# Performance work log

Measured on AMD Instinct MI355X. Metric: run time of the kernel, lower is better.

The kernel has to match this reference:

```python
import jax, jax.numpy as jnp
import numpy as np

N = 4096
NFEAT = 256
NHID1 = 64
NHID2 = 32
NCLASS = 8
NHEADS = 4
NADJ = 2
ALPHA = 0.2  # leaky relu slope
NEG = -9e15


def setup_inputs() -> dict:
    key = jax.random.key(0)
    ks = jax.random.split(key, 14)
    x = jax.random.normal(ks[0], (N, NFEAT), jnp.float32)
    adj = (jax.random.uniform(ks[1], (NADJ, N, N)) < 0.01).astype(jnp.float32)
    adj = jnp.maximum(adj, jnp.eye(N, dtype=jnp.float32)[None])
    s = 0.05
    W1 = jax.random.normal(ks[2], (NADJ, NHEADS, NFEAT, NHID1), jnp.float32) * s
    a1 = jax.random.normal(ks[3], (NADJ, NHEADS, 2, NHID1), jnp.float32) * s
    W2 = jax.random.normal(ks[4], (NADJ, NHEADS, NHID1, NHID2), jnp.float32) * s
    a2 = jax.random.normal(ks[5], (NADJ, NHEADS, 2, NHID2), jnp.float32) * s
    Wi1 = jax.random.normal(ks[6], (NHID1 * NHEADS, NHID1), jnp.float32) * s
    bi1 = jnp.zeros((NHID1,), jnp.float32)
    Wi2 = jax.random.normal(ks[7], (NHID2 * NHEADS, NCLASS), jnp.float32) * s
    bi2 = jnp.zeros((NCLASS,), jnp.float32)
    Wf = jax.random.normal(ks[8], (NCLASS * NADJ, NCLASS), jnp.float32) * s
    bf = jnp.zeros((NCLASS,), jnp.float32)
    return {"x": x, "adj": adj, "W1": W1, "a1": a1, "W2": W2, "a2": a2,
            "Wi1": Wi1, "bi1": bi1, "Wi2": Wi2, "bi2": bi2, "Wf": Wf, "bf": bf}


def gat_multihead(x, adj_i, W, a):
    # x: [n, f]; adj_i: [n, n]; W: [h, f, o]; a: [h, 2, o]
    Wh = jnp.einsum('nf,hfo->hno', x, W)                 # [h, n, o]
    f_src = jnp.einsum('hno,ho->hn', Wh, a[:, 0])        # [h, n]
    f_dst = jnp.einsum('hno,ho->hn', Wh, a[:, 1])        # [h, n]
    e = jax.nn.leaky_relu(f_src[:, :, None] + f_dst[:, None, :], ALPHA)
    e = jnp.where(adj_i[None] > 0, e, NEG)               # masked scores [h, n, n]
    att = jax.nn.softmax(e, axis=-1)
    h = jnp.einsum('hnm,hmo->hno', att, Wh)              # aggregate
    h = jax.nn.elu(h)                                     # concat=True -> elu
    n = x.shape[0]
    return jnp.transpose(h, (1, 0, 2)).reshape(n, -1)     # [n, h*o]


def reference(x, adj, W1, a1, W2, a2, Wi1, bi1, Wi2, bi2, Wf, bf):
    outs = []
    for i in range(NADJ):  # small fixed loop over adjacency graphs
        xi = gat_multihead(x, adj[i], W1[i], a1[i])
        xi = jax.nn.elu(xi @ Wi1 + bi1)
        xi = gat_multihead(xi, adj[i], W2[i], a2[i])
        xi = jax.nn.elu(xi @ Wi2 + bi2)
        outs.append(xi)
    out = jnp.concatenate(outs, axis=1) @ Wf + bf         # [n, nclass]
    l1_loss = jnp.mean(jnp.abs(Wf))
    return jax.nn.log_softmax(out, axis=1), l1_loss
```

## Files before the change

### kernel.cpp

```cpp
#include <hip/hip_runtime.h>
#include <hip/hip_bf16.h>

#define NN 4096
#define NFEAT 256
#define NHID1 64
#define NHID2 32
#define NCLASS 8
#define NHEADS 4
#define NADJ 2
#define CAP 128

__global__ __launch_bounds__(256) void build_edges(const float* __restrict__ adj,
                                                   int* __restrict__ eidx,
                                                   int* __restrict__ ecnt) {
  const int wave = threadIdx.x >> 6;
  const int lane = threadIdx.x & 63;
  const int r = blockIdx.x * 4 + wave;
  const float4* row = (const float4*)(adj + (size_t)r * NN);
  int* out = eidx + (size_t)r * CAP;
  int base = 0;
  for (int c = 0; c < NN; c += 256) {
    const float4 v = row[(c >> 2) + lane];
    const int j0 = c + lane * 4;
    const float vt[4] = {v.x, v.y, v.z, v.w};
#pragma unroll
    for (int t = 0; t < 4; ++t) {
      const bool hit = vt[t] > 0.f;
      const unsigned long long m = __ballot(hit);
      if (hit) {
        const int pos = base + __popcll(m & ((1ull << lane) - 1ull));
        if (pos < CAP) out[pos] = j0 + t;
      }
      base += __popcll(m);
    }
  }
  if (lane == 0) ecnt[r] = base < CAP ? base : CAP;
}

template <int KDIM, int NDIM, int RPTY, int ACT, int COEF>
__global__ __launch_bounds__(256) void gemm_tile(
    const float* __restrict__ A, const float* __restrict__ B,
    const float* __restrict__ bias, float* __restrict__ C,
    const float* __restrict__ av, float* __restrict__ fsrc,
    float* __restrict__ fdst,
    size_t asG, size_t bsH, size_t bsG, size_t csH, size_t csG) {
  constexpr int KT = 32;
  constexpr int TX = NDIM / 4;
  constexpr int TY = 256 / TX;
  constexpr int BR = TY * RPTY;
  const int g = blockIdx.z, h = blockIdx.y;
  const int gh = g * NHEADS + h;
  A += (size_t)g * asG;
  B += (size_t)g * bsG + (size_t)h * bsH;
  C += (size_t)g * csG + (size_t)h * csH;
  __shared__ float AsT[KT][BR + 4];
  __shared__ float Bs[KT][NDIM + 4];
  const int tid = threadIdx.x;
  const int tx = tid % TX, ty = tid / TX;
  const int row0b = blockIdx.x * BR;
  const int c0 = tx * 4;
  float acc[RPTY][4];
#pragma unroll
  for (int i = 0; i < RPTY; ++i)
#pragma unroll
    for (int j = 0; j < 4; ++j) acc[i][j] = 0.f;

  for (int kt = 0; kt < KDIM; kt += KT) {
    __syncthreads();
    for (int i = tid; i < BR * (KT / 4); i += 256) {
      const int r = i / (KT / 4), e = i % (KT / 4);
      const float4 v = *(const float4*)(A + (size_t)(row0b + r) * KDIM + kt + e * 4);
      AsT[e * 4 + 0][r] = v.x;
      AsT[e * 4 + 1][r] = v.y;
      AsT[e * 4 + 2][r] = v.z;
      AsT[e * 4 + 3][r] = v.w;
    }
    for (int i = tid; i < KT * (NDIM / 4); i += 256) {
      const int k = i / (NDIM / 4), cc = i % (NDIM / 4);
      *(float4*)&Bs[k][cc * 4] = *(const float4*)(B + (size_t)(kt + k) * NDIM + cc * 4);
    }
    __syncthreads();
#pragma unroll
    for (int k = 0; k < KT; ++k) {
      float a4[RPTY];
      if constexpr (RPTY == 4) {
        const float4 t = *(const float4*)&AsT[k][ty * 4];
        a4[0] = t.x; a4[1] = t.y; a4[2] = t.z; a4[3] = t.w;
      } else {
        const float2 t = *(const float2*)&AsT[k][ty * 2];
        a4[0] = t.x; a4[1] = t.y;
      }
      const float4 bv = *(const float4*)&Bs[k][c0];
      const float b4[4] = {bv.x, bv.y, bv.z, bv.w};
#pragma unroll
      for (int i = 0; i < RPTY; ++i)
#pragma unroll
        for (int j = 0; j < 4; ++j) acc[i][j] += a4[i] * b4[j];
    }
  }
  float b4[4] = {0.f, 0.f, 0.f, 0.f};
  if (bias) {
    const float4 bb = *(const float4*)&bias[c0];
    b4[0] = bb.x; b4[1] = bb.y; b4[2] = bb.z; b4[3] = bb.w;
  }
#pragma unroll
  for (int i = 0; i < RPTY; ++i) {
    const int row = row0b + ty * RPTY + i;
    float4 o;
    float* op = (float*)&o;
#pragma unroll
    for (int j = 0; j < 4; ++j) {
      float v = acc[i][j] + b4[j];
      if (ACT == 1) v = v > 0.f ? v : (__expf(v) - 1.f);
      op[j] = v;
    }
    *(float4*)&C[(size_t)row * NDIM + c0] = o;
  }
  if constexpr (COEF) {
    const float* ag = av + (size_t)gh * 2 * NDIM;
    float aS[4], aD[4];
#pragma unroll
    for (int j = 0; j < 4; ++j) { aS[j] = ag[c0 + j]; aD[j] = ag[NDIM + c0 + j]; }
#pragma unroll
    for (int i = 0; i < RPTY; ++i) {
      float s = 0.f, d = 0.f;
#pragma unroll
      for (int j = 0; j < 4; ++j) { s += acc[i][j] * aS[j]; d += acc[i][j] * aD[j]; }
#pragma unroll
      for (int off = TX / 2; off; off >>= 1) {
        s += __shfl_xor(s, off);
        d += __shfl_xor(d, off);
      }
      if (tx == 0) {
        const int row = row0b + ty * RPTY + i;
        fsrc[(size_t)gh * NN + row] = s;
        fdst[(size_t)gh * NN + row] = d;
      }
    }
  }
}

template <int O>
__global__ __launch_bounds__(256) void aggregate(const float* __restrict__ Wh,
                                                 const float* __restrict__ fsrc,
                                                 const float* __restrict__ fdst,
                                                 const int* __restrict__ eidx,
                                                 const int* __restrict__ ecnt,
                                                 float* __restrict__ Hout) {
  constexpr int EPI = 64 / O;
  __shared__ float wgt[4][CAP];
  __shared__ int midx[4][CAP];
  const int wave = threadIdx.x >> 6;
  const int lane = threadIdx.x & 63;
  const int n = blockIdx.x * 4 + wave;
  const int h = blockIdx.y, g = blockIdx.z;
  const int gh = g * NHEADS + h;
  Wh += (size_t)gh * NN * O;
  const int cnt = ecnt[(size_t)g * NN + n];
  const int* ei = eidx + (size_t)(g * NN + n) * CAP;
  const float fs = fsrc[(size_t)gh * NN + n];
  const float* fd = fdst + (size_t)gh * NN;
  float mx = -3.4e38f;
  for (int j = lane; j < cnt; j += 64) {
    const int m = ei[j];
    float e = fs + fd[m];
    e = e > 0.f ? e : 0.2f * e;
    midx[wave][j] = m;
    wgt[wave][j] = e;
    mx = fmaxf(mx, e);
  }
  for (int off = 32; off; off >>= 1) mx = fmaxf(mx, __shfl_xor(mx, off));
  float sm = 0.f;
  for (int j = lane; j < cnt; j += 64) {
    const float w = __expf(wgt[wave][j] - mx);
    wgt[wave][j] = w;
    sm += w;
  }
  for (int off = 32; off; off >>= 1) sm += __shfl_xor(sm, off);
  const int eo = lane / O;
  const int o = lane % O;
  float a0 = 0.f, a1 = 0.f, a2 = 0.f, a3 = 0.f;
  int j = eo;
  for (; j + 3 * EPI < cnt; j += 4 * EPI) {
    a0 += wgt[wave][j] * Wh[(size_t)midx[wave][j] * O + o];
    a1 += wgt[wave][j + EPI] * Wh[(size_t)midx[wave][j + EPI] * O + o];
    a2 += wgt[wave][j + 2 * EPI] * Wh[(size_t)midx[wave][j + 2 * EPI] * O + o];
    a3 += wgt[wave][j + 3 * EPI] * Wh[(size_t)midx[wave][j + 3 * EPI] * O + o];
  }
  for (; j < cnt; j += EPI)
    a0 += wgt[wave][j] * Wh[(size_t)midx[wave][j] * O + o];
  float acc = (a0 + a1) + (a2 + a3);
  if (EPI == 2) acc += __shfl_xor(acc, 32);
  if (lane < O) {
    float r = acc / sm;
    r = r > 0.f ? r : (__expf(r) - 1.f);
    Hout[(size_t)g * NN * (NHEADS * O) + (size_t)n * (NHEADS * O) + h * O + lane] = r;
  }
}

__global__ __launch_bounds__(256) void tail_fused(const float* __restrict__ h2,
                                                  const float* __restrict__ Wi2,
                                                  const float* __restrict__ bi2,
                                                  const float* __restrict__ Wf,
                                                  const float* __restrict__ bfv,
                                                  float* __restrict__ out) {
  constexpr int K = NHEADS * NHID2;
  __shared__ float A0[16][K + 4];
  __shared__ float A1[16][K + 4];
  __shared__ float Bs[K][NCLASS];
  __shared__ float WfS[2 * NCLASS][NCLASS];
  __shared__ float cat[16][2 * NCLASS + 1];
  const int tid = threadIdx.x;
  const int row0 = blockIdx.x * 16;
  for (int i = tid; i < 16 * (K / 4); i += 256) {
    const int r = i >> 5, e = i & 31;
    *(float4*)&A0[r][e * 4] = *(const float4*)(h2 + (size_t)(row0 + r) * K + e * 4);
    *(float4*)&A1[r][e * 4] =
        *(const float4*)(h2 + (size_t)NN * K + (size_t)(row0 + r) * K + e * 4);
  }
  ((float4*)Bs)[tid] = ((const float4*)Wi2)[tid];
  if (tid < 32) ((float4*)WfS)[tid] = ((const float4*)Wf)[tid];
  __syncthreads();
  const int c = tid & 7;
  const int kk = (tid >> 3) & 1;
  const int r = tid >> 4;
  float s0 = kk ? 0.f : bi2[c], s1 = kk ? 0.f : bi2[c];
#pragma unroll 8
  for (int k = kk * (K / 2); k < (kk + 1) * (K / 2); ++k) {
    s0 += A0[r][k] * Bs[k][c];
    s1 += A1[r][k] * Bs[k][c];
  }
  s0 += __shfl_xor(s0, 8);
  s1 += __shfl_xor(s1, 8);
  if (kk == 0) {
    cat[r][c] = s0 > 0.f ? s0 : (__expf(s0) - 1.f);
    cat[r][NCLASS + c] = s1 > 0.f ? s1 : (__expf(s1) - 1.f);
  }
  __syncthreads();
  float logit = bfv[c];
#pragma unroll
  for (int k = 0; k < 2 * NCLASS; ++k) logit += cat[r][k] * WfS[k][c];
  float m = logit;
#pragma unroll
  for (int off = 4; off; off >>= 1) m = fmaxf(m, __shfl_xor(m, off));
  float s = __expf(logit - m);
#pragma unroll
  for (int off = 4; off; off >>= 1) s += __shfl_xor(s, off);
  if (kk == 0) out[(size_t)(row0 + r) * NCLASS + c] = logit - (logf(s) + m);
  if (blockIdx.x == 0 && tid < 64) {
    float v = fabsf(Wf[tid]) + fabsf(Wf[64 + tid]);
    for (int off = 32; off; off >>= 1) v += __shfl_xor(v, off);
    if (tid == 0) out[NN * NCLASS] = v * (1.f / (2 * NCLASS * NCLASS));
  }
}

extern "C" void kernel_launch(void* const* d_in, const int* in_sizes, int n_in,
                              void* d_out, int out_size, void* d_ws, size_t ws_size,
                              hipStream_t stream) {
  const float* x = (const float*)d_in[0];
  const float* adj = (const float*)d_in[1];
  const float* W1 = (const float*)d_in[2];
  const float* a1 = (const float*)d_in[3];
  const float* W2 = (const float*)d_in[4];
  const float* a2 = (const float*)d_in[5];
  const float* Wi1 = (const float*)d_in[6];
  const float* bi1 = (const float*)d_in[7];
  const float* Wi2 = (const float*)d_in[8];
  const float* bi2 = (const float*)d_in[9];
  const float* Wf = (const float*)d_in[10];
  const float* bfv = (const float*)d_in[11];
  float* out = (float*)d_out;

  char* ws = (char*)d_ws;
  int* eidx = (int*)ws;     ws += (size_t)NADJ * NN * CAP * 4;
  int* ecnt = (int*)ws;     ws += (size_t)NADJ * NN * 4;
  float* Wh1 = (float*)ws;  ws += (size_t)NADJ * NHEADS * NN * NHID1 * 4;
  float* fs1 = (float*)ws;  ws += (size_t)NADJ * NHEADS * NN * 4;
  float* fd1 = (float*)ws;  ws += (size_t)NADJ * NHEADS * NN * 4;
  float* h1 = (float*)ws;   ws += (size_t)NADJ * NN * NHEADS * NHID1 * 4;
  float* x1 = (float*)ws;   ws += (size_t)NADJ * NN * NHID1 * 4;
  float* Wh2 = (float*)ws;  ws += (size_t)NADJ * NHEADS * NN * NHID2 * 4;
  float* fs2 = (float*)ws;  ws += (size_t)NADJ * NHEADS * NN * 4;
  float* fd2 = (float*)ws;  ws += (size_t)NADJ * NHEADS * NN * 4;
  float* h2 = (float*)ws;   ws += (size_t)NADJ * NN * NHEADS * NHID2 * 4;

  build_edges<<<NADJ * NN / 4, 256, 0, stream>>>(adj, eidx, ecnt);

  gemm_tile<NFEAT, NHID1, 4, 0, 1><<<dim3(NN / 64, NHEADS, NADJ), 256, 0, stream>>>(
      x, W1, nullptr, Wh1, a1, fs1, fd1,
      0, (size_t)NFEAT * NHID1, (size_t)NHEADS * NFEAT * NHID1,
      (size_t)NN * NHID1, (size_t)NHEADS * NN * NHID1);
  aggregate<NHID1><<<dim3(NN / 4, NHEADS, NADJ), 256, 0, stream>>>(
      Wh1, fs1, fd1, eidx, ecnt, h1);
  gemm_tile<NHEADS * NHID1, NHID1, 2, 1, 0><<<dim3(NN / 32, 1, NADJ), 256, 0, stream>>>(
      h1, Wi1, bi1, x1, nullptr, nullptr, nullptr,
      (size_t)NN * NHEADS * NHID1, 0, 0, 0, (size_t)NN * NHID1);

  gemm_tile<NHID1, NHID2, 4, 0, 1><<<dim3(NN / 128, NHEADS, NADJ), 256, 0, stream>>>(
      x1, W2, nullptr, Wh2, a2, fs2, fd2,
      (size_t)NN * NHID1, (size_t)NHID1 * NHID2, (size_t)NHEADS * NHID1 * NHID2,
      (size_t)NN * NHID2, (size_t)NHEADS * NN * NHID2);
  aggregate<NHID2><<<dim3(NN / 4, NHEADS, NADJ), 256, 0, stream>>>(
      Wh2, fs2, fd2, eidx, ecnt, h2);

  tail_fused<<<NN / 16, 256, 0, stream>>>(h2, Wi2, bi2, Wf, bfv, out);
}
```

Before: 122.4 us.

## Merge edge-list build with first GEMM and vectorize aggregate gathers to float4

The adjacency compaction and the first per-head projection GEMM, which are independent, now run as one launch. Block indices below the GEMM count do the tiled GEMM and the remaining blocks scan adjacency rows, so the two overlap and one launch is saved. The aggregate kernel now gathers neighbor feature rows as float4 per lane, with several edges handled per wave in parallel and then combined by shuffle, instead of scalar loads. In exchange, the fused kernel mixes uneven block types, and the aggregate needs extra shuffle reductions.

```diff
diff --git a/kernel.cpp b/kernel.cpp
--- a/kernel.cpp
+++ b/kernel.cpp
@@ -10,31 +10,145 @@
 #define NADJ 2
 #define CAP 128
 
-__global__ __launch_bounds__(256) void build_edges(const float* __restrict__ adj,
-                                                   int* __restrict__ eidx,
-                                                   int* __restrict__ ecnt) {
-  const int wave = threadIdx.x >> 6;
-  const int lane = threadIdx.x & 63;
-  const int r = blockIdx.x * 4 + wave;
-  const float4* row = (const float4*)(adj + (size_t)r * NN);
-  int* out = eidx + (size_t)r * CAP;
-  int base = 0;
-  for (int c = 0; c < NN; c += 256) {
-    const float4 v = row[(c >> 2) + lane];
-    const int j0 = c + lane * 4;
-    const float vt[4] = {v.x, v.y, v.z, v.w};
-#pragma unroll
-    for (int t = 0; t < 4; ++t) {
-      const bool hit = vt[t] > 0.f;
-      const unsigned long long m = __ballot(hit);
-      if (hit) {
-        const int pos = base + __popcll(m & ((1ull << lane) - 1ull));
-        if (pos < CAP) out[pos] = j0 + t;
+template <int KDIM, int NDIM, int RPTY, int ACT, int COEF>
+__device__ __forceinline__ void gemm_body(
+    const float* __restrict__ A, const float* __restrict__ B,
+    const float* __restrict__ bias, float* __restrict__ C,
+    const float* __restrict__ ag, float* __restrict__ fsrc,
+    float* __restrict__ fdst, const int row0b,
+    float* __restrict__ sA, float* __restrict__ sB) {
+  constexpr int KT = 32;
+  constexpr int TX = NDIM / 4;
+  constexpr int TY = 256 / TX;
+  constexpr int BR = TY * RPTY;
+  constexpr int LDA = BR + 4;
+  constexpr int LDB = NDIM + 4;
+  const int tid = threadIdx.x;
+  const int tx = tid % TX, ty = tid / TX;
+  const int c0 = tx * 4;
+  float acc[RPTY][4];
+#pragma unroll
+  for (int i = 0; i < RPTY; ++i)
+#pragma unroll
+    for (int j = 0; j < 4; ++j) acc[i][j] = 0.f;
+
+  for (int kt = 0; kt < KDIM; kt += KT) {
+    __syncthreads();
+    for (int i = tid; i < BR * (KT / 4); i += 256) {
+      const int r = i / (KT / 4), e = i % (KT / 4);
+      const float4 v = *(const float4*)(A + (size_t)(row0b + r) * KDIM + kt + e * 4);
+      sA[(e * 4 + 0) * LDA + r] = v.x;
+      sA[(e * 4 + 1) * LDA + r] = v.y;
+      sA[(e * 4 + 2) * LDA + r] = v.z;
+      sA[(e * 4 + 3) * LDA + r] = v.w;
+    }
+    for (int i = tid; i < KT * (NDIM / 4); i += 256) {
+      const int k = i / (NDIM / 4), cc = i % (NDIM / 4);
+      *(float4*)&sB[k * LDB + cc * 4] = *(const float4*)(B + (size_t)(kt + k) * NDIM + cc * 4);
+    }
+    __syncthreads();
+#pragma unroll
+    for (int k = 0; k < KT; ++k) {
+      float a4[RPTY];
+      if constexpr (RPTY == 4) {
+        const float4 t = *(const float4*)&sA[k * LDA + ty * 4];
+        a4[0] = t.x; a4[1] = t.y; a4[2] = t.z; a4[3] = t.w;
+      } else {
+        const float2 t = *(const float2*)&sA[k * LDA + ty * 2];
+        a4[0] = t.x; a4[1] = t.y;
       }
-      base += __popcll(m);
-    }
-  }
-  if (lane == 0) ecnt[r] = base < CAP ? base : CAP;
+      const float4 bv = *(const float4*)&sB[k * LDB + c0];
+      const float b4[4] = {bv.x, bv.y, bv.z, bv.w};
+#pragma unroll
+      for (int i = 0; i < RPTY; ++i)
+#pragma unroll
+        for (int j = 0; j < 4; ++j) acc[i][j] += a4[i] * b4[j];
+    }
+  }
+  float b4[4] = {0.f, 0.f, 0.f, 0.f};
+  if (bias) {
+    const float4 bb = *(const float4*)&bias[c0];
+    b4[0] = bb.x; b4[1] = bb.y; b4[2] = bb.z; b4[3] = bb.w;
+  }
+#pragma unroll
+  for (int i = 0; i < RPTY; ++i) {
+    const int row = row0b + ty * RPTY + i;
+    float4 o;
+    float* op = (float*)&o;
+#pragma unroll
+    for (int j = 0; j < 4; ++j) {
+      float v = acc[i][j] + b4[j];
+      if (ACT == 1) v = v > 0.f ? v : (__expf(v) - 1.f);
+      op[j] = v;
+    }
+    *(float4*)&C[(size_t)row * NDIM + c0] = o;
+  }
+  if constexpr (COEF) {
+    float aS[4], aD[4];
+#pragma unroll
+    for (int j = 0; j < 4; ++j) { aS[j] = ag[c0 + j]; aD[j] = ag[NDIM + c0 + j]; }
+#pragma unroll
+    for (int i = 0; i < RPTY; ++i) {
+      float s = 0.f, d = 0.f;
+#pragma unroll
+      for (int j = 0; j < 4; ++j) { s += acc[i][j] * aS[j]; d += acc[i][j] * aD[j]; }
+#pragma unroll
+      for (int off = TX / 2; off; off >>= 1) {
+        s += __shfl_xor(s, off);
+        d += __shfl_xor(d, off);
+      }
+      if (tx == 0) {
+        const int row = row0b + ty * RPTY + i;
+        fsrc[row] = s;
+        fdst[row] = d;
+      }
+    }
+  }
+}
+
+__global__ __launch_bounds__(256) void k1_gemm_edges(
+    const float* __restrict__ x, const float* __restrict__ W1,
+    const float* __restrict__ a1, float* __restrict__ Wh1,
+    float* __restrict__ fs1, float* __restrict__ fd1,
+    const float* __restrict__ adj, int* __restrict__ eidx,
+    int* __restrict__ ecnt) {
+  __shared__ float sA[32 * (64 + 4)];
+  __shared__ float sB[32 * (64 + 4)];
+  constexpr int NB_GEMM = (NN / 64) * NHEADS * NADJ;
+  if (blockIdx.x < NB_GEMM) {
+    int b = blockIdx.x;
+    const int tile = b % (NN / 64); b /= (NN / 64);
+    const int h = b % NHEADS;
+    const int g = b / NHEADS;
+    const int gh = g * NHEADS + h;
+    gemm_body<NFEAT, NHID1, 4, 0, 1>(
+        x, W1 + (size_t)gh * NFEAT * NHID1, nullptr,
+        Wh1 + (size_t)gh * NN * NHID1, a1 + (size_t)gh * 2 * NHID1,
+        fs1 + (size_t)gh * NN, fd1 + (size_t)gh * NN, tile * 64, sA, sB);
+  } else {
+    const int wave = threadIdx.x >> 6;
+    const int lane = threadIdx.x & 63;
+    const int r = (blockIdx.x - NB_GEMM) * 4 + wave;
+    const float4* row = (const float4*)(adj + (size_t)r * NN);
+    int* out = eidx + (size_t)r * CAP;
+    int base = 0;
+    for (int c = 0; c < NN; c += 256) {
+      const float4 v = row[(c >> 2) + lane];
+      const int j0 = c + lane * 4;
+      const float vt[4] = {v.x, v.y, v.z, v.w};
+#pragma unroll
+      for (int t = 0; t < 4; ++t) {
+        const bool hit = vt[t] > 0.f;
+        const unsigned long long m = __ballot(hit);
+        if (hit) {
+          const int pos = base + __popcll(m & ((1ull << lane) - 1ull));
+          if (pos < CAP) out[pos] = j0 + t;
+        }
+        base += __popcll(m);
+      }
+    }
+    if (lane == 0) ecnt[r] = base < CAP ? base : CAP;
+  }
 }
 
 template <int KDIM, int NDIM, int RPTY, int ACT, int COEF>
@@ -44,101 +158,29 @@
     const float* __restrict__ av, float* __restrict__ fsrc,
     float* __restrict__ fdst,
     size_t asG, size_t bsH, size_t bsG, size_t csH, size_t csG) {
-  constexpr int KT = 32;
   constexpr int TX = NDIM / 4;
   constexpr int TY = 256 / TX;
   constexpr int BR = TY * RPTY;
+  __shared__ float sA[32 * (BR + 4)];
+  __shared__ float sB[32 * (NDIM + 4)];
   const int g = blockIdx.z, h = blockIdx.y;
   const int gh = g * NHEADS + h;
-  A += (size_t)g * asG;
-  B += (size_t)g * bsG + (size_t)h * bsH;
-  C += (size_t)g * csG + (size_t)h * csH;
-  __shared__ float AsT[KT][BR + 4];
-  __shared__ float Bs[KT][NDIM + 4];
-  const int tid = threadIdx.x;
-  const int tx = tid % TX, ty = tid / TX;
-  const int row0b = blockIdx.x * BR;
-  const int c0 = tx * 4;
-  float acc[RPTY][4];
-#pragma unroll
-  for (int i = 0; i < RPTY; ++i)
-#pragma unroll
-    for (int j = 0; j < 4; ++j) acc[i][j] = 0.f;
-
-  for (int kt = 0; kt < KDIM; kt += KT) {
-    __syncthreads();
-    for (int i = tid; i < BR * (KT / 4); i += 256) {
-      const int r = i / (KT / 4), e = i % (KT / 4);
-      const float4 v = *(const float4*)(A + (size_t)(row0b + r) * KDIM + kt + e * 4);
-      AsT[e * 4 + 0][r] = v.x;
-      AsT[e * 4 + 1][r] = v.y;
-      AsT[e * 4 + 2][r] = v.z;
-      AsT[e * 4 + 3][r] = v.w;
-    }
-    for (int i = tid; i < KT * (NDIM / 4); i += 256) {
-      const int k = i / (NDIM / 4), cc = i % (NDIM / 4);
-      *(float4*)&Bs[k][cc * 4] = *(const float4*)(B + (size_t)(kt + k) * NDIM + cc * 4);
-    }
-    __syncthreads();
-#pragma unroll
-    for (int k = 0; k < KT; ++k) {
-      float a4[RPTY];
-      if constexpr (RPTY == 4) {
-        const float4 t = *(const float4*)&AsT[k][ty * 4];
-        a4[0] = t.x; a4[1] = t.y; a4[2] = t.z; a4[3] = t.w;
-      } else {
-        const float2 t = *(const float2*)&AsT[k][ty * 2];
-        a4[0] = t.x; a4[1] = t.y;
-      }
-      const float4 bv = *(const float4*)&Bs[k][c0];
-      const float b4[4] = {bv.x, bv.y, bv.z, bv.w};
-#pragma unroll
-      for (int i = 0; i < RPTY; ++i)
-#pragma unroll
-        for (int j = 0; j < 4; ++j) acc[i][j] += a4[i] * b4[j];
-    }
-  }
-  float b4[4] = {0.f, 0.f, 0.f, 0.f};
-  if (bias) {
-    const float4 bb = *(const float4*)&bias[c0];
-    b4[0] = bb.x; b4[1] = bb.y; b4[2] = bb.z; b4[3] = bb.w;
-  }
-#pragma unroll
-  for (int i = 0; i < RPTY; ++i) {
-    const int row = row0b + ty * RPTY + i;
-    float4 o;
-    float* op = (float*)&o;
-#pragma unroll
-    for (int j = 0; j < 4; ++j) {
-      float v = acc[i][j] + b4[j];
-      if (ACT == 1) v = v > 0.f ? v : (__expf(v) - 1.f);
-      op[j] = v;
-    }
-    *(float4*)&C[(size_t)row * NDIM + c0] = o;
-  }
-  if constexpr (COEF) {
-    const float* ag = av + (size_t)gh * 2 * NDIM;
-    float aS[4], aD[4];
-#pragma unroll
-    for (int j = 0; j < 4; ++j) { aS[j] = ag[c0 + j]; aD[j] = ag[NDIM + c0 + j]; }
-#pragma unroll
-    for (int i = 0; i < RPTY; ++i) {
-      float s = 0.f, d = 0.f;
-#pragma unroll
-      for (int j = 0; j < 4; ++j) { s += acc[i][j] * aS[j]; d += acc[i][j] * aD[j]; }
-#pragma unroll
-      for (int off = TX / 2; off; off >>= 1) {
-        s += __shfl_xor(s, off);
-        d += __shfl_xor(d, off);
-      }
-      if (tx == 0) {
-        const int row = row0b + ty * RPTY + i;
-        fsrc[(size_t)gh * NN + row] = s;
-        fdst[(size_t)gh * NN + row] = d;
-      }
-    }
-  }
-}
+  gemm_body<KDIM, NDIM, RPTY, ACT, COEF>(
+      A + (size_t)g * asG, B + (size_t)g * bsG + (size_t)h * bsH, bias,
+      C + (size_t)g * csG + (size_t)h * csH,
+      COEF ? av + (size_t)gh * 2 * NDIM : nullptr,
+      COEF ? fsrc + (size_t)gh * NN : nullptr,
+      COEF ? fdst + (size_t)gh * NN : nullptr,
+      (int)blockIdx.x * BR, sA, sB);
+}
+
+#define GATHER(ACC, JJ)                                                     \
+  do {                                                                      \
+    const float w_ = wgt[wave][JJ];                                         \
+    const float4 v_ = *(const float4*)(Wh + (size_t)midx[wave][JJ] * O + c4); \
+    ACC.x += w_ * v_.x; ACC.y += w_ * v_.y;                                 \
+    ACC.z += w_ * v_.z; ACC.w += w_ * v_.w;                                 \
+  } while (0)
 
 template <int O>
 __global__ __launch_bounds__(256) void aggregate(const float* __restrict__ Wh,
@@ -147,7 +189,8 @@
                                                  const int* __restrict__ eidx,
                                                  const int* __restrict__ ecnt,
                                                  float* __restrict__ Hout) {
-  constexpr int EPI = 64 / O;
+  constexpr int CPL = O / 4;
+  constexpr int EPW = 64 / CPL;
   __shared__ float wgt[4][CAP];
   __shared__ int midx[4][CAP];
   const int wave = threadIdx.x >> 6;
@@ -177,24 +220,39 @@
     sm += w;
   }
   for (int off = 32; off; off >>= 1) sm += __shfl_xor(sm, off);
-  const int eo = lane / O;
-  const int o = lane % O;
-  float a0 = 0.f, a1 = 0.f, a2 = 0.f, a3 = 0.f;
-  int j = eo;
-  for (; j + 3 * EPI < cnt; j += 4 * EPI) {
-    a0 += wgt[wave][j] * Wh[(size_t)midx[wave][j] * O + o];
-    a1 += wgt[wave][j + EPI] * Wh[(size_t)midx[wave][j + EPI] * O + o];
-    a2 += wgt[wave][j + 2 * EPI] * Wh[(size_t)midx[wave][j + 2 * EPI] * O + o];
-    a3 += wgt[wave][j + 3 * EPI] * Wh[(size_t)midx[wave][j + 3 * EPI] * O + o];
-  }
-  for (; j < cnt; j += EPI)
-    a0 += wgt[wave][j] * Wh[(size_t)midx[wave][j] * O + o];
-  float acc = (a0 + a1) + (a2 + a3);
-  if (EPI == 2) acc += __shfl_xor(acc, 32);
-  if (lane < O) {
-    float r = acc / sm;
-    r = r > 0.f ? r : (__expf(r) - 1.f);
-    Hout[(size_t)g * NN * (NHEADS * O) + (size_t)n * (NHEADS * O) + h * O + lane] = r;
+  const int sub = lane / CPL;
+  const int c4 = (lane % CPL) * 4;
+  float4 a0 = {0, 0, 0, 0}, a1 = {0, 0, 0, 0}, a2 = {0, 0, 0, 0}, a3 = {0, 0, 0, 0};
+  int j = sub;
+  for (; j + 3 * EPW < cnt; j += 4 * EPW) {
+    GATHER(a0, j);
+    GATHER(a1, j + EPW);
+    GATHER(a2, j + 2 * EPW);
+    GATHER(a3, j + 3 * EPW);
+  }
+  for (; j < cnt; j += EPW) GATHER(a0, j);
+  float4 acc;
+  acc.x = (a0.x + a1.x) + (a2.x + a3.x);
+  acc.y = (a0.y + a1.y) + (a2.y + a3.y);
+  acc.z = (a0.z + a1.z) + (a2.z + a3.z);
+  acc.w = (a0.w + a1.w) + (a2.w + a3.w);
+#pragma unroll
+  for (int off = CPL; off < 64; off <<= 1) {
+    acc.x += __shfl_xor(acc.x, off);
+    acc.y += __shfl_xor(acc.y, off);
+    acc.z += __shfl_xor(acc.z, off);
+    acc.w += __shfl_xor(acc.w, off);
+  }
+  if (lane < CPL) {
+    const float inv = 1.f / sm;
+    float4 o;
+    o.x = acc.x * inv; o.y = acc.y * inv; o.z = acc.z * inv; o.w = acc.w * inv;
+    o.x = o.x > 0.f ? o.x : (__expf(o.x) - 1.f);
+    o.y = o.y > 0.f ? o.y : (__expf(o.y) - 1.f);
+    o.z = o.z > 0.f ? o.z : (__expf(o.z) - 1.f);
+    o.w = o.w > 0.f ? o.w : (__expf(o.w) - 1.f);
+    *(float4*)&Hout[(size_t)g * NN * (NHEADS * O) + (size_t)n * (NHEADS * O) +
+                    h * O + c4] = o;
   }
 }
 
@@ -284,14 +342,12 @@
   float* fd2 = (float*)ws;  ws += (size_t)NADJ * NHEADS * NN * 4;
   float* h2 = (float*)ws;   ws += (size_t)NADJ * NN * NHEADS * NHID2 * 4;
 
-  build_edges<<<NADJ * NN / 4, 256, 0, stream>>>(adj, eidx, ecnt);
-
-  gemm_tile<NFEAT, NHID1, 4, 0, 1><<<dim3(NN / 64, NHEADS, NADJ), 256, 0, stream>>>(
-      x, W1, nullptr, Wh1, a1, fs1, fd1,
-      0, (size_t)NFEAT * NHID1, (size_t)NHEADS * NFEAT * NHID1,
-      (size_t)NN * NHID1, (size_t)NHEADS * NN * NHID1);
+  k1_gemm_edges<<<512 + NADJ * NN / 4, 256, 0, stream>>>(
+      x, W1, a1, Wh1, fs1, fd1, adj, eidx, ecnt);
+
   aggregate<NHID1><<<dim3(NN / 4, NHEADS, NADJ), 256, 0, stream>>>(
       Wh1, fs1, fd1, eidx, ecnt, h1);
+
   gemm_tile<NHEADS * NHID1, NHID1, 2, 1, 0><<<dim3(NN / 32, 1, NADJ), 256, 0, stream>>>(
       h1, Wi1, bi1, x1, nullptr, nullptr, nullptr,
       (size_t)NN * NHEADS * NHID1, 0, 0, 0, (size_t)NN * NHID1);
@@ -300,6 +356,7 @@
       x1, W2, nullptr, Wh2, a2, fs2, fd2,
       (size_t)NN * NHID1, (size_t)NHID1 * NHID2, (size_t)NHEADS * NHID1 * NHID2,
       (size_t)NN * NHID2, (size_t)NHEADS * NN * NHID2);
+
   aggregate<NHID2><<<dim3(NN / 4, NHEADS, NADJ), 256, 0, stream>>>(
       Wh2, fs2, fd2, eidx, ecnt, h2);
 
```

New measurement: 101.3 us. 17.2% less time.
